# Performance work log

Hardware: AMD Instinct MI355X
Metric: run time of the kernel (lower is better)

## Reference

```python
import jax, jax.numpy as jnp
import numpy as np

EPS = 1e-7  # keras backend epsilon
B, D_IN, H, L, DEPTH = 16384, 784, 512, 32, 2

def _lrelu(x):
    return jax.nn.leaky_relu(x, 0.3)  # tf.keras LeakyReLU default alpha

def _router(h, W1, b1, W2, b2, W3, b3):
    h = _lrelu(h @ W1 + b1)
    h = _lrelu(h @ W2 + b2)
    return jax.nn.sigmoid((h @ W3 + b3)[:, 0])

def setup_inputs():
    key = jax.random.key(0)
    ks = jax.random.split(key, 20)
    s = 0.02
    n = lambda k, sh: jax.random.normal(k, sh, jnp.float32) * s
    return {
        'x': jax.random.uniform(ks[0], (B, D_IN), jnp.float32),
        'enc_W0': n(ks[1], (D_IN, H)), 'enc_b0': jnp.zeros((H,), jnp.float32),
        'enc_W': n(ks[2], (3, H, H)), 'enc_b': jnp.zeros((3, H), jnp.float32),
        'dense_Wmu': n(ks[3], (7, H, L)), 'dense_bmu': jnp.zeros((7, L), jnp.float32),
        'dense_Wsig': n(ks[4], (7, H, L)), 'dense_bsig': jnp.zeros((7, L), jnp.float32),
        'trans_Wh': n(ks[5], (6, L, H)), 'trans_bh': jnp.zeros((6, H), jnp.float32),
        'trans_Wmu': n(ks[6], (6, H, L)), 'trans_bmu': jnp.zeros((6, L), jnp.float32),
        'trans_Wsig': n(ks[7], (6, H, L)), 'trans_bsig': jnp.zeros((6, L), jnp.float32),
        'routp_W1': n(ks[8], (3, L, H)), 'routp_b1': jnp.zeros((3, H), jnp.float32),
        'routp_W2': n(ks[9], (3, H, H)), 'routp_b2': jnp.zeros((3, H), jnp.float32),
        'routp_W3': n(ks[10], (3, H, 1)), 'routp_b3': jnp.zeros((3, 1), jnp.float32),
        'routq_W1': n(ks[11], (3, H, H)), 'routq_b1': jnp.zeros((3, H), jnp.float32),
        'routq_W2': n(ks[12], (3, H, H)), 'routq_b2': jnp.zeros((3, H), jnp.float32),
        'routq_W3': n(ks[13], (3, H, 1)), 'routq_b3': jnp.zeros((3, 1), jnp.float32),
        'dec_W1': n(ks[14], (4, L, H)), 'dec_b1': jnp.zeros((4, H), jnp.float32),
        'dec_W2': n(ks[15], (4, H, D_IN)), 'dec_b2': jnp.zeros((4, D_IN), jnp.float32),
    }

def reference(x, enc_W0, enc_b0, enc_W, enc_b,
              dense_Wmu, dense_bmu, dense_Wsig, dense_bsig,
              trans_Wh, trans_bh, trans_Wmu, trans_bmu, trans_Wsig, trans_bsig,
              routp_W1, routp_b1, routp_W2, routp_b2, routp_W3, routp_b3,
              routq_W1, routq_b1, routq_W2, routq_b2, routq_W3, routq_b3,
              dec_W1, dec_b1, dec_W2, dec_b2):
    Bn = x.shape[0]
    # bottom-up encoder chain; encoders collects layers i >= len - (depth+1) = 1
    d = _lrelu(x @ enc_W0 + enc_b0)
    encoders = []
    for i in range(3):
        d = _lrelu(d @ enc_W[i] + enc_b[i])
        encoders.append(d)
    depth_of = [0, 1, 1, 2, 2, 2, 2]  # BFS depth of the 7 tree nodes
    probs = {0: jnp.ones((Bn,), x.dtype)}
    zs = {}
    kl_nodes_tot = jnp.zeros((Bn,), x.dtype)
    kl_dec_tot = jnp.zeros((Bn,), x.dtype)
    kl_root = None
    leaves_prob, recons = [], []
    base = jax.random.key(1)
    for k in range(7):
        dl = depth_of[k]
        d = encoders[DEPTH - dl]
        mu_q_hat = d @ dense_Wmu[k] + dense_bmu[k]
        sig_q_hat = jax.nn.softplus(d @ dense_Wsig[k] + dense_bsig[k])
        if k == 0:
            mu_p = jnp.zeros_like(mu_q_hat)
            sig_p = jnp.ones_like(sig_q_hat)
            mu_q, sig_q = mu_q_hat, sig_q_hat
        else:
            zp = zs[(k - 1) // 2]
            h = _lrelu(zp @ trans_Wh[k - 1] + trans_bh[k - 1])
            mu_p = h @ trans_Wmu[k - 1] + trans_bmu[k - 1]
            sig_p = jax.nn.softplus(h @ trans_Wsig[k - 1] + trans_bsig[k - 1])
            # compute_posterior: precision-weighted fusion
            sig_q = 1.0 / (1.0 / sig_q_hat + 1.0 / sig_p)
            mu_q = sig_q * (mu_q_hat / sig_q_hat + mu_p / sig_p)
        vq = sig_q + EPS
        vp = sig_p + EPS
        # KL(N(mu_q, vq) || N(mu_p, vp)) for diag Gaussians (scale = sqrt(sigma+eps))
        kl = 0.5 * jnp.sum(vq / vp + (mu_q - mu_p) ** 2 / vp - 1.0 + jnp.log(vp / vq), axis=1)
        kl_node = jnp.clip(probs[k] * kl, -1.0, 1000.0)
        if k == 0:
            kl_root = kl_node
        else:
            kl_nodes_tot = kl_nodes_tot + kl_node
        eps_n = jax.random.normal(jax.random.fold_in(base, k), mu_q.shape, x.dtype)
        z = mu_q + jnp.sqrt(vq) * eps_n  # reparameterized sample
        zs[k] = z
        if k < 3:  # internal node: routing
            pl = _router(z, routp_W1[k], routp_b1[k], routp_W2[k], routp_b2[k], routp_W3[k], routp_b3[k])
            plq = _router(d, routq_W1[k], routq_b1[k], routq_W2[k], routq_b2[k], routq_W3[k], routq_b3[k])
            kl_dec = plq * jnp.log(EPS + plq / (pl + EPS)) + (1.0 - plq) * jnp.log(EPS + (1.0 - plq) / (1.0 - pl + EPS))
            kl_dec_tot = kl_dec_tot + probs[k] * kl_dec
            probs[2 * k + 1] = probs[k] * plq
            probs[2 * k + 2] = probs[k] * (1.0 - plq)
        else:  # leaf: decode
            leaves_prob.append(probs[k])
            h = _lrelu(z @ dec_W1[k - 3] + dec_b1[k - 3])
            recons.append(jax.nn.sigmoid(h @ dec_W2[k - 3] + dec_b2[k - 3]))
    rec_losses = jnp.zeros((Bn,), x.dtype)
    for p, r in zip(leaves_prob, recons):
        bce = -jnp.sum(x * jnp.log(r + EPS) + (1.0 - x) * jnp.log(1.0 - r + EPS), axis=1)
        rec_losses = rec_losses + p * bce
    # elbo_samples, per-sample total loss (shape [B])
    return kl_nodes_tot + kl_dec_tot + kl_root + rec_losses
```

## Files before the change

### kernel.cpp

```cpp
#include <hip/hip_runtime.h>
#include <cstdint>
#include <cstddef>

#define B_ROWS 16384
#define DIN 784
#define HD 512
#define LD 32

typedef __attribute__((ext_vector_type(8))) short short8;
typedef __attribute__((ext_vector_type(4))) float f32x4;
typedef __attribute__((ext_vector_type(4))) unsigned short us4;

struct I4 { int x, y, z, w; };
__device__ inline int i4get(I4 v, int z) { return z == 0 ? v.x : z == 1 ? v.y : z == 2 ? v.z : v.w; }

__device__ inline unsigned short f2bf(float v) {
  union { float f; unsigned u; } x; x.f = v;
  unsigned r = x.u + 0x7fffu + ((x.u >> 16) & 1u);
  return (unsigned short)(r >> 16);
}
__device__ inline float bf2f(unsigned short b) {
  union { unsigned u; float f; } x; x.u = ((unsigned)b) << 16;
  return x.f;
}

__host__ __device__ inline void threefry2x32(uint32_t k0, uint32_t k1,
                                             uint32_t x0, uint32_t x1,
                                             uint32_t& o0, uint32_t& o1) {
  uint32_t ks2 = k0 ^ k1 ^ 0x1BD11BDAu;
#define TF_ROT(x, d) (((x) << (d)) | ((x) >> (32 - (d))))
#define TF_R(r) { x0 += x1; x1 = TF_ROT(x1, r); x1 ^= x0; }
  x0 += k0; x1 += k1;
  TF_R(13) TF_R(15) TF_R(26) TF_R(6)
  x0 += k1; x1 += ks2 + 1u;
  TF_R(17) TF_R(29) TF_R(16) TF_R(24)
  x0 += ks2; x1 += k0 + 2u;
  TF_R(13) TF_R(15) TF_R(26) TF_R(6)
  x0 += k0; x1 += k1 + 3u;
  TF_R(17) TF_R(29) TF_R(16) TF_R(24)
  x0 += k1; x1 += ks2 + 4u;
  TF_R(13) TF_R(15) TF_R(26) TF_R(6)
  x0 += ks2; x1 += k0 + 5u;
  o0 = x0; o1 = x1;
#undef TF_R
#undef TF_ROT
}

__device__ inline float erfinv_f(float x) {
  float w = -log1pf(-x * x);
  float p;
  if (w < 5.0f) {
    w -= 2.5f;
    p = 2.81022636e-08f;
    p = fmaf(p, w, 3.43273939e-07f);
    p = fmaf(p, w, -3.5233877e-06f);
    p = fmaf(p, w, -4.39150654e-06f);
    p = fmaf(p, w, 0.00021858087f);
    p = fmaf(p, w, -0.00125372503f);
    p = fmaf(p, w, -0.00417768164f);
    p = fmaf(p, w, 0.246640727f);
    p = fmaf(p, w, 1.50140941f);
  } else {
    w = sqrtf(w) - 3.0f;
    p = -0.000200214257f;
    p = fmaf(p, w, 0.000100950558f);
    p = fmaf(p, w, 0.00134934322f);
    p = fmaf(p, w, -0.00367342844f);
    p = fmaf(p, w, 0.00573950773f);
    p = fmaf(p, w, -0.0076224613f);
    p = fmaf(p, w, 0.00943887047f);
    p = fmaf(p, w, 1.00167406f);
    p = fmaf(p, w, 2.83297682f);
  }
  return p * x;
}

__device__ inline float jax_normal_elem(uint32_t ka, uint32_t kb, uint32_t idx) {
  uint32_t b1, b2;
  threefry2x32(ka, kb, 0u, idx, b1, b2);
  uint32_t bits = b1 ^ b2;
  uint32_t fb = (bits >> 9) | 0x3f800000u;
  float f = __uint_as_float(fb) - 1.0f;
  const float lo = -0.99999994f;
  float u = f * 2.0f + lo;
  u = fmaxf(u, lo);
  return 1.41421356f * erfinv_f(u);
}

struct WJob {
  unsigned short pi;
  unsigned src_off, dst_off, start;
  short K, N, Np, Kp;
};
struct WJobs { WJob j[56]; unsigned total; };

constexpr WJobs make_jobs() {
  WJobs W{};
  int idx = 0; unsigned start = 0; unsigned d = 0;
  auto add = [&](int pi, unsigned so, int K, int N, int Np, int Kp, unsigned doff) {
    W.j[idx].pi = (unsigned short)pi; W.j[idx].src_off = so; W.j[idx].dst_off = doff;
    W.j[idx].start = start; W.j[idx].K = (short)K; W.j[idx].N = (short)N;
    W.j[idx].Np = (short)Np; W.j[idx].Kp = (short)Kp;
    start += (unsigned)(Np * Kp); ++idx;
  };
  add(0, 0, 784, 512, 512, 832, d); d += 512 * 832;
  for (int i = 0; i < 3; ++i) { add(1, i * 262144u, 512, 512, 512, 512, d); d += 262144; }
  for (int k = 0; k < 7; ++k) { add(2, k * 16384u, 512, 32, 32, 512, d);
                                add(3, k * 16384u, 512, 32, 32, 512, d + 16384); d += 32768; }
  for (int i = 0; i < 6; ++i) { add(4, i * 16384u, 32, 512, 512, 32, d); d += 16384; }
  for (int i = 0; i < 6; ++i) { add(5, i * 16384u, 512, 32, 32, 512, d);
                                add(6, i * 16384u, 512, 32, 32, 512, d + 16384); d += 32768; }
  for (int k = 0; k < 3; ++k) { add(7, k * 16384u, 32, 512, 512, 32, d); d += 16384; }
  for (int k = 0; k < 3; ++k) { add(8, k * 262144u, 512, 512, 512, 512, d); d += 262144; }
  for (int k = 0; k < 3; ++k) { add(9, k * 262144u, 512, 512, 512, 512, d); d += 262144; }
  for (int k = 0; k < 3; ++k) { add(10, k * 262144u, 512, 512, 512, 512, d); d += 262144; }
  for (int i = 0; i < 4; ++i) { add(11, i * 16384u, 32, 512, 512, 32, d); d += 16384; }
  for (int i = 0; i < 4; ++i) { add(12, i * 401408u, 512, 784, 896, 512, d); d += 458752; }
  W.total = start;
  return W;
}
__device__ constexpr WJobs g_jobs = make_jobs();

struct TileTable { unsigned ts[57]; };
constexpr TileTable make_tiles() {
  TileTable T{}; WJobs J = make_jobs();
  unsigned acc = 0;
  for (int i = 0; i < 56; ++i) {
    T.ts[i] = acc;
    acc += (unsigned)(J.j[i].Np / 32) * (unsigned)(J.j[i].Kp / 32);
  }
  T.ts[56] = acc;
  return T;
}
__device__ constexpr TileTable g_tiles = make_tiles();

#define OFF_ENC0T 0u
#define OFF_ENCT 425984u
#define OFF_DENSE 1212416u
#define OFF_TWH 1441792u
#define OFF_TMS 1540096u
#define OFF_RP1 1736704u
#define OFF_RP2 1785856u
#define OFF_RQ1 2572288u
#define OFF_RQ2 3358720u
#define OFF_DC1 4145152u
#define OFF_DC2 4210688u
#define ARENA_ELEMS 6045696u

struct WSrcs { const float* p[13]; };

__global__ void wconv_k(WSrcs srcs, unsigned short* __restrict__ arena) {
  __shared__ unsigned short tile[32][34];
  unsigned bid = blockIdx.x;
  int jo = 0;
#pragma unroll 1
  while (jo + 1 < 56 && g_tiles.ts[jo + 1] <= bid) ++jo;
  const WJob J = g_jobs.j[jo];
  unsigned t = bid - g_tiles.ts[jo];
  unsigned ktiles = (unsigned)J.Kp / 32u;
  unsigned n0 = (t / ktiles) * 32u, k0 = (t % ktiles) * 32u;
  int ty = threadIdx.x >> 3, tx4 = (threadIdx.x & 7) * 4;
  float v0 = 0, v1 = 0, v2 = 0, v3 = 0;
  int kk = (int)k0 + ty;
  if (kk < J.K) {
    const float* sp = srcs.p[J.pi] + J.src_off + (size_t)kk * J.N + n0 + tx4;
    int nb = (int)(n0 + tx4);
    if (nb + 3 < J.N) {
      float4 v = *reinterpret_cast<const float4*>(sp);
      v0 = v.x; v1 = v.y; v2 = v.z; v3 = v.w;
    } else {
      if (nb + 0 < J.N) v0 = sp[0];
      if (nb + 1 < J.N) v1 = sp[1];
      if (nb + 2 < J.N) v2 = sp[2];
      if (nb + 3 < J.N) v3 = sp[3];
    }
  }
  tile[tx4 + 0][ty] = f2bf(v0);
  tile[tx4 + 1][ty] = f2bf(v1);
  tile[tx4 + 2][ty] = f2bf(v2);
  tile[tx4 + 3][ty] = f2bf(v3);
  __syncthreads();
  us4 w;
  w.x = tile[ty][tx4 + 0]; w.y = tile[ty][tx4 + 1];
  w.z = tile[ty][tx4 + 2]; w.w = tile[ty][tx4 + 3];
  *reinterpret_cast<us4*>(&arena[J.dst_off + (size_t)(n0 + ty) * J.Kp + k0 + tx4]) = w;
}

__global__ void xconv_k(const float* __restrict__ x, unsigned short* __restrict__ xb832,
                        unsigned short* __restrict__ xb784) {
  unsigned g = blockIdx.x * 256u + threadIdx.x;
  unsigned r = g / 208u, c4 = g % 208u;
  unsigned c = c4 * 4u;
  float v0 = 0, v1 = 0, v2 = 0, v3 = 0;
  if (c + 3 < 784u) {
    float4 v = *reinterpret_cast<const float4*>(x + (size_t)r * 784u + c);
    v0 = v.x; v1 = v.y; v2 = v.z; v3 = v.w;
  } else {
    if (c + 0 < 784u) v0 = x[(size_t)r * 784u + c + 0];
    if (c + 1 < 784u) v1 = x[(size_t)r * 784u + c + 1];
    if (c + 2 < 784u) v2 = x[(size_t)r * 784u + c + 2];
    if (c + 3 < 784u) v3 = x[(size_t)r * 784u + c + 3];
  }
  us4 w; w.x = f2bf(v0); w.y = f2bf(v1); w.z = f2bf(v2); w.w = f2bf(v3);
  *reinterpret_cast<us4*>(&xb832[(size_t)r * 832u + c]) = w;
  if (c + 3 < 784u)
    *reinterpret_cast<us4*>(&xb784[(size_t)r * 784u + c]) = w;
}

template <int BM, int BN, int BK, int NW, int DB, int ACT, typename OT>
__global__ __launch_bounds__(NW * 64)
void mgemm_k(const unsigned short* __restrict__ A, int sA,
             const unsigned short* __restrict__ Wt,
             const float* __restrict__ b1, const float* __restrict__ b2,
             OT* __restrict__ C, int sC, int Nreal, int K,
             I4 zAo, I4 zWo, I4 zCo, int zB1, int zB2,
             const unsigned short* __restrict__ xx) {
  constexpr int WCN = NW / 2;
  constexpr int WN = BN / WCN;
  constexpr int NF = WN / 16;
  constexpr int MR = BM / 2 / 16;
  constexpr int KS = BK / 32;
  constexpr int LPR = BK / 8;
  constexpr int RPC = 64 / LPR;
  constexpr int CA = BM / RPC, CB = BN / RPC;
  constexpr int CAW = (CA >= NW) ? CA / NW : 1;
  constexpr int CBW = (CB >= NW) ? CB / NW : 1;
  constexpr int LPW = CAW + CBW;
  __shared__ unsigned short As[DB][BM][BK];
  __shared__ unsigned short Bs[DB][BN][BK];
  __shared__ float sums[BM][WCN];

  int bx, by, bz;
  {
    const int nx = gridDim.x, ny = gridDim.y;
    const int L = blockIdx.x + nx * (blockIdx.y + ny * blockIdx.z);
    const int xw = nx >> 3;
    const int xcd = L & 7, i = L >> 3;
    bx = xcd * xw + i % xw;
    const int rest = i / xw;
    by = rest % ny;
    bz = rest / ny;
  }

  A += i4get(zAo, bz);
  Wt += i4get(zWo, bz);
  C += i4get(zCo, bz);
  b1 += (size_t)bz * zB1;
  if (ACT == 3 || ACT == 4) { if (b2) b2 += (size_t)bz * zB2; }

  const int tid = threadIdx.x;
  const int lane = tid & 63;
  const int wid = tid >> 6;
  const int wr = wid / WCN, wc = wid % WCN;
  const int bm = bx * BM;
  const int bn = by * BN;
  const int lr = lane / LPR;
  const int lk = (BK == 32) ? (((lane & 3) ^ ((lane >> 3) & 3)) * 8)
                            : ((lane % LPR) * 8);

  auto stage = [&](int buf, int k0) {
#pragma unroll
    for (int cc = 0; cc < CAW; ++cc) {
      int c = wid * CAW + cc;
      if (CAW * NW == CA || c < CA) {
        const unsigned short* g = A + (size_t)(bm + c * RPC + lr) * sA + k0 + lk;
        __builtin_amdgcn_global_load_lds(
            (const __attribute__((address_space(1))) void*)g,
            (__attribute__((address_space(3))) void*)(&As[buf][c * RPC][0]), 16, 0, 0);
      }
    }
#pragma unroll
    for (int cc = 0; cc < CBW; ++cc) {
      int c = wid * CBW + cc;
      if (CBW * NW == CB || c < CB) {
        const unsigned short* g = Wt + (size_t)(bn + c * RPC + lr) * K + k0 + lk;
        __builtin_amdgcn_global_load_lds(
            (const __attribute__((address_space(1))) void*)g,
            (__attribute__((address_space(3))) void*)(&Bs[buf][c * RPC][0]), 16, 0, 0);
      }
    }
  };

  f32x4 acc[MR][NF];
#pragma unroll
  for (int m = 0; m < MR; ++m)
#pragma unroll
    for (int n = 0; n < NF; ++n) acc[m][n] = (f32x4){0.f, 0.f, 0.f, 0.f};

  const int ar = wr * (BM / 2) + (lane & 15);
  const int ac = (BK == 32) ? ((((lane >> 4) ^ ((lane >> 1) & 3)) & 3) * 8)
                            : ((lane >> 4) * 8);
  const int br = wc * WN + (lane & 15);
  const int nt = K / BK;

  auto compute = [&](int buf) {
    short8 aF[MR][KS], bF[NF][KS];
#pragma unroll
    for (int m = 0; m < MR; ++m)
#pragma unroll
      for (int kk = 0; kk < KS; ++kk)
        aF[m][kk] = *reinterpret_cast<const short8*>(&As[buf][ar + m * 16][ac + kk * 32]);
#pragma unroll
    for (int n = 0; n < NF; ++n)
#pragma unroll
      for (int kk = 0; kk < KS; ++kk)
        bF[n][kk] = *reinterpret_cast<const short8*>(&Bs[buf][br + n * 16][ac + kk * 32]);
#pragma unroll
    for (int kk = 0; kk < KS; ++kk)
#pragma unroll
      for (int m = 0; m < MR; ++m)
#pragma unroll
        for (int n = 0; n < NF; ++n)
          acc[m][n] = __builtin_amdgcn_mfma_f32_16x16x32_bf16(aF[m][kk], bF[n][kk], acc[m][n], 0, 0, 0);
  };

  if constexpr (DB >= 2) {
    stage(0, 0);
    if (DB >= 3 && nt > 1) stage(1, BK);
    for (int t = 0; t < nt; ++t) {
      const int pf = t + DB - 1;
      if (pf < nt) stage(pf % DB, pf * BK);
      int ahead = nt - 1 - t; if (ahead > DB - 1) ahead = DB - 1;
      const int w = ahead * LPW;
      if (w >= 8)      asm volatile("s_waitcnt vmcnt(8)" ::: "memory");
      else if (w == 6) asm volatile("s_waitcnt vmcnt(6)" ::: "memory");
      else if (w == 4) asm volatile("s_waitcnt vmcnt(4)" ::: "memory");
      else if (w == 3) asm volatile("s_waitcnt vmcnt(3)" ::: "memory");
      else if (w == 2) asm volatile("s_waitcnt vmcnt(2)" ::: "memory");
      else             asm volatile("s_waitcnt vmcnt(0)" ::: "memory");
      __builtin_amdgcn_s_barrier();
      asm volatile("" ::: "memory");
      compute(t % DB);
      asm volatile("" ::: "memory");
      __builtin_amdgcn_s_barrier();
      asm volatile("" ::: "memory");
    }
  } else {
    for (int t = 0; t < nt; ++t) {
      stage(0, t * BK);
      __syncthreads();
      compute(0);
      __syncthreads();
    }
  }

  if constexpr (ACT == 4 || ACT == 5) {
    const int row0 = bm + wr * (BM / 2) + (lane >> 4) * 4;
#pragma unroll
    for (int m = 0; m < MR; ++m) {
#pragma unroll
      for (int r = 0; r < 4; ++r) {
        float s = 0.0f;
        int grow = row0 + m * 16 + r;
#pragma unroll
        for (int n = 0; n < NF; ++n) {
          int col = bn + wc * WN + n * 16 + (lane & 15);
          float v = acc[m][n][r];
          if constexpr (ACT == 4) {
            v += b1[col];
            v = (v >= 0.0f) ? v : 0.3f * v;
            s += v * b2[col];
          } else {
            if (col < Nreal) {
              v += b1[col];
              float sp = fmaxf(v, 0.0f) + __logf(1.0f + __expf(-fabsf(v)));
              float xv = bf2f(xx[(size_t)grow * Nreal + col]);
              s += fmaf(xv, v, -sp);
            }
          }
        }
#pragma unroll
        for (int msk = 1; msk < 16; msk <<= 1) s += __shfl_xor(s, msk, 64);
        if ((lane & 15) == 0) sums[wr * (BM / 2) + m * 16 + (lane >> 4) * 4 + r][wc] = s;
      }
    }
    __syncthreads();
    if (tid < BM) {
      float t = 0.0f;
#pragma unroll
      for (int wv = 0; wv < WCN; ++wv) t += sums[tid][wv];
      float* Cf = (float*)C;
      Cf[(size_t)(bm + tid) * sC + by] = t;
    }
  } else {
#pragma unroll
    for (int m = 0; m < MR; ++m) {
      int row = bm + wr * (BM / 2) + m * 16 + (lane >> 4) * 4;
#pragma unroll
      for (int n = 0; n < NF; ++n) {
        int col = bn + wc * WN + n * 16 + (lane & 15);
        if (col < Nreal) {
#pragma unroll
          for (int r = 0; r < 4; ++r) {
            float v = acc[m][n][r];
            if constexpr (ACT == 3) {
              int nl = col >> 6, cin = col & 63;
              if (cin < 32) {
                v += b1[nl * 32 + cin];
              } else {
                v += b2[nl * 32 + (cin - 32)];
                v = fmaxf(v, 0.0f) + log1pf(__expf(-fabsf(v)));
              }
            } else {
              v += b1[col];
              if (ACT == 1) v = (v >= 0.0f) ? v : 0.3f * v;
            }
            size_t oidx = (size_t)(row + r) * sC + col;
            if constexpr (sizeof(OT) == 2) C[oidx] = (OT)f2bf(v);
            else C[oidx] = (OT)v;
          }
        }
      }
    }
  }
}

struct Keys { uint32_t a[7]; uint32_t b[7]; };

__global__ void node_k(int kstart, Keys keys,
                       const float* __restrict__ musigAll,
                       const float* __restrict__ mupsigAll,
                       const float* __restrict__ probs,
                       unsigned short* __restrict__ zbuf,
                       float* __restrict__ contrib) {
  const int knode = kstart + blockIdx.y;
  const int row = blockIdx.x * 8 + (threadIdx.x >> 5);
  const int j = threadIdx.x & 31;
  const float* mq = musigAll + (size_t)row * 448 + 64 * knode;
  float mqh = mq[j], sqh = mq[32 + j];
  float mu_q, sig_q, mu_p, sig_p;
  if (knode == 0) {
    mu_p = 0.0f; sig_p = 1.0f; mu_q = mqh; sig_q = sqh;
  } else {
    const float* mp = mupsigAll + (size_t)row * 448 + 64 * knode;
    mu_p = mp[j]; sig_p = mp[32 + j];
    sig_q = 1.0f / (1.0f / sqh + 1.0f / sig_p);
    mu_q = sig_q * (mqh / sqh + mu_p / sig_p);
  }
  float vq = sig_q + 1e-7f, vp = sig_p + 1e-7f;
  float dm = mu_q - mu_p;
  float kj = vq / vp + dm * dm / vp - 1.0f + logf(vp / vq);
#pragma unroll
  for (int msk = 1; msk < 32; msk <<= 1) kj += __shfl_xor(kj, msk, 64);
  float e = jax_normal_elem(keys.a[knode], keys.b[knode], (uint32_t)(row * 32 + j));
  zbuf[(size_t)knode * B_ROWS * 32 + (size_t)row * 32 + j] = f2bf(mu_q + sqrtf(vq) * e);
  if (j == 0) {
    float p = (knode == 0) ? 1.0f : probs[(size_t)knode * B_ROWS + row];
    float kn = fminf(fmaxf(p * 0.5f * kj, -1.0f), 1000.0f);
    contrib[(size_t)knode * B_ROWS + row] = kn;
  }
}

__global__ void route_k(int kstart, const float* __restrict__ plp,
                        const float* __restrict__ plqp,
                        const float* __restrict__ rpb3, const float* __restrict__ rqb3,
                        float* __restrict__ probs, float* __restrict__ contrib) {
  const int k = kstart + blockIdx.y;
  const int row = blockIdx.x * 256 + threadIdx.x;
  const float* pp = plp + ((size_t)k * B_ROWS + row) * 4;
  const float* pq = plqp + ((size_t)k * B_ROWS + row) * 4;
  float sl = pp[0] + pp[1] + pp[2] + pp[3];
  float sq = pq[0] + pq[1] + pq[2] + pq[3];
  float pl = 1.0f / (1.0f + expf(-(sl + rpb3[k])));
  float plq = 1.0f / (1.0f + expf(-(sq + rqb3[k])));
  float p = (k == 0) ? 1.0f : probs[(size_t)k * B_ROWS + row];
  float kld = plq * logf(1e-7f + plq / (pl + 1e-7f)) +
              (1.0f - plq) * logf(1e-7f + (1.0f - plq) / (1.0f - pl + 1e-7f));
  contrib[(size_t)(7 + k) * B_ROWS + row] = p * kld;
  probs[(size_t)(2 * k + 1) * B_ROWS + row] = p * plq;
  probs[(size_t)(2 * k + 2) * B_ROWS + row] = p * (1.0f - plq);
}

__global__ void final_k(const float* __restrict__ contrib, const float* __restrict__ probs,
                        const float* __restrict__ pbce, float* __restrict__ out) {
  const int row = blockIdx.x * 256 + threadIdx.x;
  float s = 0.0f;
#pragma unroll
  for (int i = 0; i < 10; ++i) s += contrib[(size_t)i * B_ROWS + row];
#pragma unroll
  for (int l = 0; l < 4; ++l) {
    const float* pb = pbce + ((size_t)l * B_ROWS + row) * 7;
    float bs = 0.0f;
#pragma unroll
    for (int y = 0; y < 7; ++y) bs += pb[y];
    s += probs[(size_t)(3 + l) * B_ROWS + row] * (-bs);
  }
  out[row] = s;
}

extern "C" void kernel_launch(void* const* d_in, const int* in_sizes, int n_in,
                              void* d_out, int out_size, void* d_ws, size_t ws_size,
                              hipStream_t stream) {
  const float* x      = (const float*)d_in[0];
  const float* enc_W0 = (const float*)d_in[1];
  const float* enc_b0 = (const float*)d_in[2];
  const float* enc_W  = (const float*)d_in[3];
  const float* enc_b  = (const float*)d_in[4];
  const float* dWmu   = (const float*)d_in[5];
  const float* dbmu   = (const float*)d_in[6];
  const float* dWsig  = (const float*)d_in[7];
  const float* dbsig  = (const float*)d_in[8];
  const float* tWh    = (const float*)d_in[9];
  const float* tbh    = (const float*)d_in[10];
  const float* tWmu   = (const float*)d_in[11];
  const float* tbmu   = (const float*)d_in[12];
  const float* tWsig  = (const float*)d_in[13];
  const float* tbsig  = (const float*)d_in[14];
  const float* rpW1   = (const float*)d_in[15];
  const float* rpb1   = (const float*)d_in[16];
  const float* rpW2   = (const float*)d_in[17];
  const float* rpb2   = (const float*)d_in[18];
  const float* rpW3   = (const float*)d_in[19];
  const float* rpb3   = (const float*)d_in[20];
  const float* rqW1   = (const float*)d_in[21];
  const float* rqb1   = (const float*)d_in[22];
  const float* rqW2   = (const float*)d_in[23];
  const float* rqb2   = (const float*)d_in[24];
  const float* rqW3   = (const float*)d_in[25];
  const float* rqb3   = (const float*)d_in[26];
  const float* dcW1   = (const float*)d_in[27];
  const float* dcb1   = (const float*)d_in[28];
  const float* dcW2   = (const float*)d_in[29];
  const float* dcb2   = (const float*)d_in[30];
  float* out = (float*)d_out;
  (void)in_sizes; (void)n_in; (void)out_size; (void)ws_size;

  const size_t BR = B_ROWS;
  unsigned short* h = (unsigned short*)d_ws;
  unsigned short* encA  = h;
  unsigned short* encB  = h + BR * 512;
  unsigned short* encC  = h + BR * 1024;
  unsigned short* bufT  = h + BR * 1536;
  unsigned short* zbuf  = h + BR * 2560;
  unsigned short* xb784 = h + BR * 2784;
  unsigned short* arena = h + BR * 3568;
  size_t ho = BR * 3568 + ARENA_ELEMS;
  float* f = (float*)(h + ho);
  float* musigAll  = f;
  float* mupsigAll = f + BR * 448;
  float* probs     = f + BR * 896;
  float* plp       = f + BR * 903;
  float* plqp      = f + BR * 915;
  float* pbce      = f + BR * 927;
  float* contrib   = f + BR * 955;
  unsigned short* xb832 = (unsigned short*)f;

  const int offA = 0;
  const int offC = (int)(BR * 1024);
  const int offT = (int)(BR * 1536);

  Keys keys;
  for (int k = 0; k < 7; ++k) threefry2x32(0u, 1u, 0u, (uint32_t)k, keys.a[k], keys.b[k]);

  const I4 Z0 = {0, 0, 0, 0};
  constexpr TileTable HT = make_tiles();

  xconv_k<<<dim3((B_ROWS * 208) / 256), 256, 0, stream>>>(x, xb832, xb784);
  WSrcs srcs;
  srcs.p[0] = enc_W0; srcs.p[1] = enc_W; srcs.p[2] = dWmu; srcs.p[3] = dWsig;
  srcs.p[4] = tWh; srcs.p[5] = tWmu; srcs.p[6] = tWsig;
  srcs.p[7] = rpW1; srcs.p[8] = rpW2; srcs.p[9] = rqW1; srcs.p[10] = rqW2;
  srcs.p[11] = dcW1; srcs.p[12] = dcW2;
  wconv_k<<<dim3(HT.ts[56]), 256, 0, stream>>>(srcs, arena);

#define LAUNCH(BN, BK, ACT, OT, A, sA, W, B1, B2, Cc, sC, Nr, K, gy, gz, zA, zW, zC, zb1, zb2, XX) \
  mgemm_k<64, BN, BK, 4, 1, ACT, OT><<<dim3(B_ROWS / 64, gy, gz), 256, 0, stream>>>( \
      A, sA, W, B1, B2, Cc, sC, Nr, K, zA, zW, zC, zb1, zb2, XX)
#define LAUNCH8(BN, BK, ACT, OT, A, sA, W, B1, B2, Cc, sC, Nr, K, gy, gz, zA, zW, zC, zb1, zb2, XX) \
  mgemm_k<128, BN, BK, 8, 2, ACT, OT><<<dim3(B_ROWS / 128, gy, gz), 512, 0, stream>>>( \
      A, sA, W, B1, B2, Cc, sC, Nr, K, zA, zW, zC, zb1, zb2, XX)

  LAUNCH8(128, 32, 1, unsigned short, xb832, 832, arena + OFF_ENC0T, enc_b0, nullptr,
          bufT, 512, 512, 832, 4, 1, Z0, Z0, Z0, 0, 0, nullptr);
  LAUNCH8(128, 32, 1, unsigned short, bufT, 512, arena + OFF_ENCT + 0u, enc_b + 0, nullptr,
          encA, 512, 512, 512, 4, 1, Z0, Z0, Z0, 0, 0, nullptr);
  LAUNCH(128, 32, 3, float, encA, 512, arena + OFF_DENSE + 3u * 32768u, dbmu + 96, dbsig + 96,
         musigAll + 192, 448, 256, 512, 2, 1, Z0, Z0, Z0, 0, 0, nullptr);
  LAUNCH8(128, 32, 1, unsigned short, encA, 512, arena + OFF_ENCT + 262144u, enc_b + 512, nullptr,
          encB, 512, 512, 512, 4, 1, Z0, Z0, Z0, 0, 0, nullptr);
  LAUNCH(128, 32, 3, float, encB, 512, arena + OFF_DENSE + 32768u, dbmu + 32, dbsig + 32,
         musigAll + 64, 448, 128, 512, 1, 1, Z0, Z0, Z0, 0, 0, nullptr);
  LAUNCH8(128, 32, 1, unsigned short, encB, 512, arena + OFF_ENCT + 524288u, enc_b + 1024, nullptr,
          encC, 512, 512, 512, 4, 1, Z0, Z0, Z0, 0, 0, nullptr);
  LAUNCH(64, 32, 3, float, encC, 512, arena + OFF_DENSE, dbmu, dbsig,
         musigAll, 448, 64, 512, 1, 1, Z0, Z0, Z0, 0, 0, nullptr);
  LAUNCH8(128, 32, 1, unsigned short, encC, 512, arena + OFF_RQ1, rqb1, nullptr,
          bufT, 512, 512, 512, 4, 1, Z0, Z0, Z0, 0, 0, nullptr);
  {
    I4 zW = {0, 262144, 0, 0}, zC = {offA, offC, 0, 0};
    LAUNCH8(128, 32, 1, unsigned short, encB, 512, arena + OFF_RQ1 + 262144u, rqb1 + 512, nullptr,
            h, 512, 512, 512, 4, 2, Z0, zW, zC, 512, 0, nullptr);
  }
  {
    I4 zA = {offT, offA, offC, 0};
    I4 zW = {0, 262144, 524288, 0};
    I4 zC = {0, (int)(BR * 4), (int)(BR * 8), 0};
    LAUNCH8(128, 32, 4, float, h, 512, arena + OFF_RQ2, rqb2, rqW3,
            plqp, 4, 512, 512, 4, 3, zA, zW, zC, 512, 512, nullptr);
  }

  node_k<<<dim3(B_ROWS / 8, 1), 256, 0, stream>>>(0, keys, musigAll, mupsigAll, probs, zbuf, contrib);
  LAUNCH(128, 32, 1, unsigned short, zbuf, 32, arena + OFF_RP1, rpb1, nullptr,
         bufT, 512, 512, 32, 4, 1, Z0, Z0, Z0, 0, 0, nullptr);
  LAUNCH8(128, 32, 4, float, bufT, 512, arena + OFF_RP2, rpb2, rpW3,
          plp, 4, 512, 512, 4, 1, Z0, Z0, Z0, 0, 0, nullptr);
  route_k<<<dim3(B_ROWS / 256, 1), 256, 0, stream>>>(0, plp, plqp, rpb3, rqb3, probs, contrib);

  LAUNCH(128, 32, 1, unsigned short, zbuf, 32, arena + OFF_TWH, tbh, nullptr,
         bufT, 1024, 1024, 32, 8, 1, Z0, Z0, Z0, 0, 0, nullptr);
  {
    I4 zA = {0, 512, 0, 0}, zW = {0, 32768, 0, 0}, zC = {0, 64, 0, 0};
    LAUNCH(64, 32, 3, float, bufT, 1024, arena + OFF_TMS, tbmu, tbsig,
           mupsigAll + 64, 448, 64, 512, 1, 2, zA, zW, zC, 32, 32, nullptr);
  }
  node_k<<<dim3(B_ROWS / 8, 2), 256, 0, stream>>>(1, keys, musigAll, mupsigAll, probs, zbuf, contrib);
  {
    I4 zA = {0, (int)(BR * 32), 0, 0}, zW = {0, 16384, 0, 0}, zC = {offA, offC, 0, 0};
    LAUNCH(128, 32, 1, unsigned short, zbuf + BR * 32, 32, arena + OFF_RP1 + 16384u, rpb1 + 512, nullptr,
           h, 512, 512, 32, 4, 2, zA, zW, zC, 512, 0, nullptr);
    I4 zA2 = {offA, offC, 0, 0}, zW2 = {0, 262144, 0, 0}, zC2 = {0, (int)(BR * 4), 0, 0};
    LAUNCH8(128, 32, 4, float, h, 512, arena + OFF_RP2 + 262144u, rpb2 + 512, rpW3 + 512,
            plp + BR * 4, 4, 512, 512, 4, 2, zA2, zW2, zC2, 512, 512, nullptr);
  }
  route_k<<<dim3(B_ROWS / 256, 2), 256, 0, stream>>>(1, plp, plqp, rpb3, rqb3, probs, contrib);

  {
    I4 zA = {0, (int)(BR * 32), 0, 0};
    I4 zW = {0, 32768, 0, 0};
    I4 zC = {0, (int)(BR * 1024), 0, 0};
    LAUNCH(128, 32, 1, unsigned short, zbuf + BR * 32, 32, arena + OFF_TWH + 32768u, tbh + 1024, nullptr,
           h, 1024, 1024, 32, 8, 2, zA, zW, zC, 1024, 0, nullptr);
    I4 zA2 = {0, 512, (int)(BR * 1024), (int)(BR * 1024 + 512)};
    I4 zW2 = {0, 32768, 65536, 98304};
    I4 zC2 = {0, 64, 128, 192};
    LAUNCH(64, 32, 3, float, h, 1024, arena + OFF_TMS + 65536u, tbmu + 64, tbsig + 64,
           mupsigAll + 192, 448, 64, 512, 1, 4, zA2, zW2, zC2, 32, 32, nullptr);
  }
  node_k<<<dim3(B_ROWS / 8, 4), 256, 0, stream>>>(3, keys, musigAll, mupsigAll, probs, zbuf, contrib);

  {
    I4 zA1 = {0, (int)(BR * 32), (int)(BR * 64), (int)(BR * 96)};
    I4 zW1 = {0, 16384, 32768, 49152};
    I4 zC1 = {0, (int)(BR * 512), (int)(BR * 1024), (int)(BR * 1536)};
    LAUNCH(128, 32, 1, unsigned short, zbuf + BR * 96, 32, arena + OFF_DC1, dcb1, nullptr,
           h, 512, 512, 32, 4, 4, zA1, zW1, zC1, 512, 0, nullptr);
    I4 zA2 = {0, (int)(BR * 512), (int)(BR * 1024), (int)(BR * 1536)};
    I4 zW2 = {0, 458752, 917504, 1376256};
    I4 zC2 = {0, (int)(BR * 7), (int)(BR * 14), (int)(BR * 21)};
    LAUNCH8(128, 32, 5, float, h, 512, arena + OFF_DC2, dcb2, nullptr,
            pbce, 7, 784, 512, 7, 4, zA2, zW2, zC2, 784, 0, xb784);
  }

  final_k<<<dim3(B_ROWS / 256), 256, 0, stream>>>(contrib, probs, pbce, out);
#undef LAUNCH
#undef LAUNCH8
}
```

Measured before the change: 564.0 us.

## Batch seven dense mu/sigma GEMMs into one launch; raise MFMA wave priority

Three separate dense-head GEMM launches that ran between the encoder layers are replaced by a single grid-z batched launch over all seven heads. Per-z A, W and C offsets now come from eight-entry offset tables. The single launch also uses a narrower BN=64 tile. The double-buffered GEMM path additionally raises wave priority around the MFMA block with s_setprio, which favours matrix issue over loads. The aim is to cut launch count and small-grid underutilisation, at the cost of delaying the dense heads until all encoders have finished and adding some per-block indexing.

```diff
diff --git a/kernel.cpp b/kernel.cpp
--- a/kernel.cpp
+++ b/kernel.cpp
@@ -13,6 +13,7 @@
 
 struct I4 { int x, y, z, w; };
 __device__ inline int i4get(I4 v, int z) { return z == 0 ? v.x : z == 1 ? v.y : z == 2 ? v.z : v.w; }
+__device__ inline int i8get(I4 lo, I4 hi, int z) { return z < 4 ? i4get(lo, z) : i4get(hi, z - 4); }
 
 __device__ inline unsigned short f2bf(float v) {
   union { float f; unsigned u; } x; x.f = v;
@@ -213,7 +214,8 @@
              const unsigned short* __restrict__ Wt,
              const float* __restrict__ b1, const float* __restrict__ b2,
              OT* __restrict__ C, int sC, int Nreal, int K,
-             I4 zAo, I4 zWo, I4 zCo, int zB1, int zB2,
+             I4 zAo, I4 zAoH, I4 zWo, I4 zWoH, I4 zCo, I4 zCoH,
+             int zB1, int zB2,
              const unsigned short* __restrict__ xx) {
   constexpr int WCN = NW / 2;
   constexpr int WN = BN / WCN;
@@ -242,9 +244,9 @@
     bz = rest / ny;
   }
 
-  A += i4get(zAo, bz);
-  Wt += i4get(zWo, bz);
-  C += i4get(zCo, bz);
+  A += i8get(zAo, zAoH, bz);
+  Wt += i8get(zWo, zWoH, bz);
+  C += i8get(zCo, zCoH, bz);
   b1 += (size_t)bz * zB1;
   if (ACT == 3 || ACT == 4) { if (b2) b2 += (size_t)bz * zB2; }
 
@@ -305,6 +307,7 @@
 #pragma unroll
       for (int kk = 0; kk < KS; ++kk)
         bF[n][kk] = *reinterpret_cast<const short8*>(&Bs[buf][br + n * 16][ac + kk * 32]);
+    if constexpr (DB >= 2) __builtin_amdgcn_s_setprio(1);
 #pragma unroll
     for (int kk = 0; kk < KS; ++kk)
 #pragma unroll
@@ -312,6 +315,7 @@
 #pragma unroll
         for (int n = 0; n < NF; ++n)
           acc[m][n] = __builtin_amdgcn_mfma_f32_16x16x32_bf16(aF[m][kk], bF[n][kk], acc[m][n], 0, 0, 0);
+    if constexpr (DB >= 2) __builtin_amdgcn_s_setprio(0);
   };
 
   if constexpr (DB >= 2) {
@@ -546,6 +550,7 @@
   unsigned short* xb832 = (unsigned short*)f;
 
   const int offA = 0;
+  const int offB = (int)(BR * 512);
   const int offC = (int)(BR * 1024);
   const int offT = (int)(BR * 1536);
 
@@ -565,25 +570,29 @@
 
 #define LAUNCH(BN, BK, ACT, OT, A, sA, W, B1, B2, Cc, sC, Nr, K, gy, gz, zA, zW, zC, zb1, zb2, XX) \
   mgemm_k<64, BN, BK, 4, 1, ACT, OT><<<dim3(B_ROWS / 64, gy, gz), 256, 0, stream>>>( \
-      A, sA, W, B1, B2, Cc, sC, Nr, K, zA, zW, zC, zb1, zb2, XX)
+      A, sA, W, B1, B2, Cc, sC, Nr, K, zA, Z0, zW, Z0, zC, Z0, zb1, zb2, XX)
 #define LAUNCH8(BN, BK, ACT, OT, A, sA, W, B1, B2, Cc, sC, Nr, K, gy, gz, zA, zW, zC, zb1, zb2, XX) \
   mgemm_k<128, BN, BK, 8, 2, ACT, OT><<<dim3(B_ROWS / 128, gy, gz), 512, 0, stream>>>( \
-      A, sA, W, B1, B2, Cc, sC, Nr, K, zA, zW, zC, zb1, zb2, XX)
+      A, sA, W, B1, B2, Cc, sC, Nr, K, zA, Z0, zW, Z0, zC, Z0, zb1, zb2, XX)
 
   LAUNCH8(128, 32, 1, unsigned short, xb832, 832, arena + OFF_ENC0T, enc_b0, nullptr,
           bufT, 512, 512, 832, 4, 1, Z0, Z0, Z0, 0, 0, nullptr);
   LAUNCH8(128, 32, 1, unsigned short, bufT, 512, arena + OFF_ENCT + 0u, enc_b + 0, nullptr,
           encA, 512, 512, 512, 4, 1, Z0, Z0, Z0, 0, 0, nullptr);
-  LAUNCH(128, 32, 3, float, encA, 512, arena + OFF_DENSE + 3u * 32768u, dbmu + 96, dbsig + 96,
-         musigAll + 192, 448, 256, 512, 2, 1, Z0, Z0, Z0, 0, 0, nullptr);
   LAUNCH8(128, 32, 1, unsigned short, encA, 512, arena + OFF_ENCT + 262144u, enc_b + 512, nullptr,
           encB, 512, 512, 512, 4, 1, Z0, Z0, Z0, 0, 0, nullptr);
-  LAUNCH(128, 32, 3, float, encB, 512, arena + OFF_DENSE + 32768u, dbmu + 32, dbsig + 32,
-         musigAll + 64, 448, 128, 512, 1, 1, Z0, Z0, Z0, 0, 0, nullptr);
   LAUNCH8(128, 32, 1, unsigned short, encB, 512, arena + OFF_ENCT + 524288u, enc_b + 1024, nullptr,
           encC, 512, 512, 512, 4, 1, Z0, Z0, Z0, 0, 0, nullptr);
-  LAUNCH(64, 32, 3, float, encC, 512, arena + OFF_DENSE, dbmu, dbsig,
-         musigAll, 448, 64, 512, 1, 1, Z0, Z0, Z0, 0, 0, nullptr);
+
+  {
+    I4 zA  = {offC, offB, offB, offA}, zAH = {offA, offA, offA, 0};
+    I4 zW  = {0, 32768, 65536, 98304}, zWH = {131072, 163840, 196608, 0};
+    I4 zC  = {0, 64, 128, 192},        zCH = {256, 320, 384, 0};
+    mgemm_k<64, 64, 32, 4, 1, 3, float><<<dim3(B_ROWS / 64, 1, 7), 256, 0, stream>>>(
+        h, 512, arena + OFF_DENSE, dbmu, dbsig, musigAll, 448, 64, 512,
+        zA, zAH, zW, zWH, zC, zCH, 32, 32, nullptr);
+  }
+
   LAUNCH8(128, 32, 1, unsigned short, encC, 512, arena + OFF_RQ1, rqb1, nullptr,
           bufT, 512, 512, 512, 4, 1, Z0, Z0, Z0, 0, 0, nullptr);
   {
```

Measured after the change: 573.4 us. About the same (+1.7%).
